# Optimization experiments

Hardware: AMD Instinct MI355X
Metric: run time of the kernel (lower is better)

The kernel has to match this reference:

```python
import jax, jax.numpy as jnp
import numpy as np

NX = NY = NZ = 192
DX = DY = DZ = 1e-3
DT = 1e-12
EPS0 = 8.8541878128e-12
MU0 = 1.25663706212e-6


def _dcentral(f, axis, inv2d):
    # central difference along `axis`, defined only on the interior of ALL
    # three dims (matches the torch edge lists built for i,j,k in 1..n-2);
    # boundary entries are zero (no scatter contributions there).
    g = jnp.zeros_like(f)
    sp = [slice(1, -1)] * 3
    sm = [slice(1, -1)] * 3
    sp[axis] = slice(2, None)
    sm[axis] = slice(0, -2)
    return g.at[1:-1, 1:-1, 1:-1].set((f[tuple(sp)] - f[tuple(sm)]) * inv2d)


def setup_inputs() -> dict:
    key = jax.random.key(0)
    ks = jax.random.split(key, 9)
    shp = (1, 1, NX, NY, NZ)
    f32 = jnp.float32
    inp = {}
    for name, k in zip(['Ex', 'Ey', 'Ez', 'Hx', 'Hy', 'Hz'], ks[:6]):
        inp[name] = jax.random.normal(k, shp, dtype=f32)
    inp['eps'] = (EPS0 * (1.0 + jax.random.uniform(ks[6], shp))).astype(f32)
    inp['mu'] = (MU0 * (1.0 + jax.random.uniform(ks[7], shp))).astype(f32)
    inp['sigma'] = (1e-3 * jax.random.uniform(ks[8], shp)).astype(f32)
    return inp


def reference(Ex, Ey, Ez, Hx, Hy, Hz, eps, mu, sigma):
    inv2dx = 1.0 / (2.0 * DX)
    inv2dy = 1.0 / (2.0 * DY)
    inv2dz = 1.0 / (2.0 * DZ)
    r3 = lambda a: a.reshape(NX, NY, NZ)  # _flatten3 equivalent layout
    ex, ey, ez = r3(Ex), r3(Ey), r3(Ez)
    hx, hy, hz = r3(Hx), r3(Hy), r3(Hz)
    eps3, mu3, sig3 = r3(eps), r3(mu), r3(sigma)

    # Step 1 (E -> H): H^{n+1/2} = H^{n-1/2} - dt/mu * curl(E^n)
    curlE_x = _dcentral(ez, 1, inv2dy) - _dcentral(ey, 2, inv2dz)
    curlE_y = _dcentral(ex, 2, inv2dz) - _dcentral(ez, 0, inv2dx)
    curlE_z = _dcentral(ey, 0, inv2dx) - _dcentral(ex, 1, inv2dy)
    hx2 = hx - (DT / mu3) * curlE_x
    hy2 = hy - (DT / mu3) * curlE_y
    hz2 = hz - (DT / mu3) * curlE_z

    # Step 2 (H -> E): E^{n+1} = (A-/A+) E^n + dt/(eps A+) * curl(H^{n+1/2})
    A_plus = 1.0 + sig3 * DT / (2.0 * eps3)
    A_minus = 1.0 - sig3 * DT / (2.0 * eps3)
    curlH_x = _dcentral(hz2, 1, inv2dy) - _dcentral(hy2, 2, inv2dz)
    curlH_y = _dcentral(hx2, 2, inv2dz) - _dcentral(hz2, 0, inv2dx)
    curlH_z = _dcentral(hy2, 0, inv2dx) - _dcentral(hx2, 1, inv2dy)
    coefE = A_minus / A_plus
    coefC = DT / (eps3 * A_plus)
    ex2 = coefE * ex + coefC * curlH_x
    ey2 = coefE * ey + coefC * curlH_y
    ez2 = coefE * ez + coefC * curlH_z

    u5 = lambda a: a.reshape(1, 1, NX, NY, NZ)  # _unflatten3
    return (u5(ex2), u5(ey2), u5(ez2), u5(hx2), u5(hy2), u5(hz2))
```

## Files before the change

kernel.cpp:

```cpp
#include <hip/hip_runtime.h>


#define NXD 192
#define NYD 192
#define NZD 192

static constexpr int   N3      = NXD * NYD * NZD;
static constexpr float DTc     = 1e-12f;
static constexpr float INV2D   = 500.0f;

static constexpr int SX = NYD * NZD;
static constexpr int SY = NZD;

__global__ __launch_bounds__(256) void fdtd_step1(
    const float* __restrict__ Ex, const float* __restrict__ Ey, const float* __restrict__ Ez,
    const float* __restrict__ Hx, const float* __restrict__ Hy, const float* __restrict__ Hz,
    const float* __restrict__ mu,
    float* __restrict__ Hx2, float* __restrict__ Hy2, float* __restrict__ Hz2)
{
    int idx = blockIdx.x * blockDim.x + threadIdx.x;
    if (idx >= N3) return;

    int k = idx % NZD;
    int t = idx / NZD;
    int j = t % NYD;
    int i = t / NYD;

    float cx = 0.0f, cy = 0.0f, cz = 0.0f;
    if (i > 0 && i < NXD - 1 && j > 0 && j < NYD - 1 && k > 0 && k < NZD - 1) {
        float dEz_dy = (Ez[idx + SY] - Ez[idx - SY]) * INV2D;
        float dEy_dz = (Ey[idx + 1 ] - Ey[idx - 1 ]) * INV2D;
        float dEx_dz = (Ex[idx + 1 ] - Ex[idx - 1 ]) * INV2D;
        float dEz_dx = (Ez[idx + SX] - Ez[idx - SX]) * INV2D;
        float dEy_dx = (Ey[idx + SX] - Ey[idx - SX]) * INV2D;
        float dEx_dy = (Ex[idx + SY] - Ex[idx - SY]) * INV2D;
        cx = dEz_dy - dEy_dz;
        cy = dEx_dz - dEz_dx;
        cz = dEy_dx - dEx_dy;
    }

    float f = DTc / mu[idx];
    Hx2[idx] = Hx[idx] - f * cx;
    Hy2[idx] = Hy[idx] - f * cy;
    Hz2[idx] = Hz[idx] - f * cz;
}

__global__ __launch_bounds__(256) void fdtd_step2(
    const float* __restrict__ Ex, const float* __restrict__ Ey, const float* __restrict__ Ez,
    const float* __restrict__ Hx2, const float* __restrict__ Hy2, const float* __restrict__ Hz2,
    const float* __restrict__ eps, const float* __restrict__ sigma,
    float* __restrict__ Ex2, float* __restrict__ Ey2, float* __restrict__ Ez2)
{
    int idx = blockIdx.x * blockDim.x + threadIdx.x;
    if (idx >= N3) return;

    int k = idx % NZD;
    int t = idx / NZD;
    int j = t % NYD;
    int i = t / NYD;

    float cx = 0.0f, cy = 0.0f, cz = 0.0f;
    if (i > 0 && i < NXD - 1 && j > 0 && j < NYD - 1 && k > 0 && k < NZD - 1) {
        float dHz_dy = (Hz2[idx + SY] - Hz2[idx - SY]) * INV2D;
        float dHy_dz = (Hy2[idx + 1 ] - Hy2[idx - 1 ]) * INV2D;
        float dHx_dz = (Hx2[idx + 1 ] - Hx2[idx - 1 ]) * INV2D;
        float dHz_dx = (Hz2[idx + SX] - Hz2[idx - SX]) * INV2D;
        float dHy_dx = (Hy2[idx + SX] - Hy2[idx - SX]) * INV2D;
        float dHx_dy = (Hx2[idx + SY] - Hx2[idx - SY]) * INV2D;
        cx = dHz_dy - dHy_dz;
        cy = dHx_dz - dHz_dx;
        cz = dHy_dx - dHx_dy;
    }

    float e  = eps[idx];
    float s  = sigma[idx];
    float half_sdt_over_e = s * DTc / (2.0f * e);
    float Ap = 1.0f + half_sdt_over_e;
    float Am = 1.0f - half_sdt_over_e;
    float coefE = Am / Ap;
    float coefC = DTc / (e * Ap);

    Ex2[idx] = coefE * Ex[idx] + coefC * cx;
    Ey2[idx] = coefE * Ey[idx] + coefC * cy;
    Ez2[idx] = coefE * Ez[idx] + coefC * cz;
}

extern "C" void kernel_launch(void* const* d_in, const int* in_sizes, int n_in,
                              void* d_out, int out_size, void* d_ws, size_t ws_size,
                              hipStream_t stream)
{
    const float* Ex    = (const float*)d_in[0];
    const float* Ey    = (const float*)d_in[1];
    const float* Ez    = (const float*)d_in[2];
    const float* Hx    = (const float*)d_in[3];
    const float* Hy    = (const float*)d_in[4];
    const float* Hz    = (const float*)d_in[5];
    const float* eps   = (const float*)d_in[6];
    const float* mu    = (const float*)d_in[7];
    const float* sigma = (const float*)d_in[8];

    float* out = (float*)d_out;
    float* Ex2 = out + 0 * (size_t)N3;
    float* Ey2 = out + 1 * (size_t)N3;
    float* Ez2 = out + 2 * (size_t)N3;
    float* Hx2 = out + 3 * (size_t)N3;
    float* Hy2 = out + 4 * (size_t)N3;
    float* Hz2 = out + 5 * (size_t)N3;

    const int block = 256;
    const int grid  = (N3 + block - 1) / block;

    fdtd_step1<<<grid, block, 0, stream>>>(Ex, Ey, Ez, Hx, Hy, Hz, mu, Hx2, Hy2, Hz2);
    fdtd_step2<<<grid, block, 0, stream>>>(Ex, Ey, Ez, Hx2, Hy2, Hz2, eps, sigma, Ex2, Ey2, Ez2);
}
```

Baseline: 379.5 us.

## Fuse H and E updates into one tiled kernel with shared-memory H halo

Merges the two stencil kernels into a single kernel where each block owns a 4x4 column tile along the full z extent. H updates for the tile plus a one-cell halo are computed into shared memory, then the E update reads curl(H) from shared memory instead of re-reading H2 from global memory. This removes the second launch and the global round-trip of the intermediate H fields, at the cost of redundant halo recomputation of H and its extra E/mu reads.

```diff
diff --git a/kernel.cpp b/kernel.cpp
--- a/kernel.cpp
+++ b/kernel.cpp
@@ -5,84 +5,148 @@
 #define NYD 192
 #define NZD 192
 
-static constexpr int   N3      = NXD * NYD * NZD;
-static constexpr float DTc     = 1e-12f;
-static constexpr float INV2D   = 500.0f;
+static constexpr int   N3    = NXD * NYD * NZD;
+static constexpr float DTc   = 1e-12f;
+static constexpr float INV2D = 500.0f;
 
 static constexpr int SX = NYD * NZD;
 static constexpr int SY = NZD;
 
-__global__ __launch_bounds__(256) void fdtd_step1(
+static constexpr int TI  = 4, TJ = 4;
+static constexpr int NTI = NXD / TI;
+static constexpr int NTJ = NYD / TJ;
+static constexpr int NT  = NTI * NTJ;
+static constexpr int BLOCK = 256;
+
+static constexpr int HZ_SZ = 6 * 6 * 192;
+static constexpr int HX_SZ = 4 * 6 * 194;
+static constexpr int HY_SZ = 6 * 4 * 194;
+
+__global__ __launch_bounds__(BLOCK, 2) void fdtd_fused(
     const float* __restrict__ Ex, const float* __restrict__ Ey, const float* __restrict__ Ez,
     const float* __restrict__ Hx, const float* __restrict__ Hy, const float* __restrict__ Hz,
-    const float* __restrict__ mu,
+    const float* __restrict__ eps, const float* __restrict__ mu, const float* __restrict__ sigma,
+    float* __restrict__ Ex2, float* __restrict__ Ey2, float* __restrict__ Ez2,
     float* __restrict__ Hx2, float* __restrict__ Hy2, float* __restrict__ Hz2)
 {
-    int idx = blockIdx.x * blockDim.x + threadIdx.x;
-    if (idx >= N3) return;
+    __shared__ float sHz[HZ_SZ];
+    __shared__ float sHx[HX_SZ];
+    __shared__ float sHy[HY_SZ];
 
-    int k = idx % NZD;
-    int t = idx / NZD;
-    int j = t % NYD;
-    int i = t / NYD;
+    unsigned b    = blockIdx.x;
+    unsigned tile = (b & 7u) * (NT / 8) + (b >> 3);
+    int ti = (int)(tile / NTJ);
+    int tj = (int)(tile % NTJ);
+    int gi0 = ti * TI;
+    int gj0 = tj * TJ;
 
-    float cx = 0.0f, cy = 0.0f, cz = 0.0f;
-    if (i > 0 && i < NXD - 1 && j > 0 && j < NYD - 1 && k > 0 && k < NZD - 1) {
-        float dEz_dy = (Ez[idx + SY] - Ez[idx - SY]) * INV2D;
-        float dEy_dz = (Ey[idx + 1 ] - Ey[idx - 1 ]) * INV2D;
-        float dEx_dz = (Ex[idx + 1 ] - Ex[idx - 1 ]) * INV2D;
-        float dEz_dx = (Ez[idx + SX] - Ez[idx - SX]) * INV2D;
-        float dEy_dx = (Ey[idx + SX] - Ey[idx - SX]) * INV2D;
-        float dEx_dy = (Ex[idx + SY] - Ex[idx - SY]) * INV2D;
-        cx = dEz_dy - dEy_dz;
-        cy = dEx_dz - dEz_dx;
-        cz = dEy_dx - dEx_dy;
+    const int tid = threadIdx.x;
+
+    for (int p = tid; p < HZ_SZ; p += BLOCK) {
+        int k  = p % 192;
+        int t  = p / 192;
+        int jj = t % 6;
+        int ii = t / 6;
+        int i = gi0 + ii - 1;
+        int j = gj0 + jj - 1;
+        if ((unsigned)i < (unsigned)NXD && (unsigned)j < (unsigned)NYD) {
+            int g = i * SX + j * SY + k;
+            float curl = 0.0f;
+            if (i > 0 && i < NXD - 1 && j > 0 && j < NYD - 1 && k > 0 && k < NZD - 1) {
+                curl = ((Ey[g + SX] - Ey[g - SX]) - (Ex[g + SY] - Ex[g - SY])) * INV2D;
+            }
+            float v = Hz[g] - (DTc / mu[g]) * curl;
+            sHz[p] = v;
+            if ((unsigned)(ii - 1) < (unsigned)TI && (unsigned)(jj - 1) < (unsigned)TJ)
+                Hz2[g] = v;
+        }
     }
 
-    float f = DTc / mu[idx];
-    Hx2[idx] = Hx[idx] - f * cx;
-    Hy2[idx] = Hy[idx] - f * cy;
-    Hz2[idx] = Hz[idx] - f * cz;
-}
-
-__global__ __launch_bounds__(256) void fdtd_step2(
-    const float* __restrict__ Ex, const float* __restrict__ Ey, const float* __restrict__ Ez,
-    const float* __restrict__ Hx2, const float* __restrict__ Hy2, const float* __restrict__ Hz2,
-    const float* __restrict__ eps, const float* __restrict__ sigma,
-    float* __restrict__ Ex2, float* __restrict__ Ey2, float* __restrict__ Ez2)
-{
-    int idx = blockIdx.x * blockDim.x + threadIdx.x;
-    if (idx >= N3) return;
-
-    int k = idx % NZD;
-    int t = idx / NZD;
-    int j = t % NYD;
-    int i = t / NYD;
-
-    float cx = 0.0f, cy = 0.0f, cz = 0.0f;
-    if (i > 0 && i < NXD - 1 && j > 0 && j < NYD - 1 && k > 0 && k < NZD - 1) {
-        float dHz_dy = (Hz2[idx + SY] - Hz2[idx - SY]) * INV2D;
-        float dHy_dz = (Hy2[idx + 1 ] - Hy2[idx - 1 ]) * INV2D;
-        float dHx_dz = (Hx2[idx + 1 ] - Hx2[idx - 1 ]) * INV2D;
-        float dHz_dx = (Hz2[idx + SX] - Hz2[idx - SX]) * INV2D;
-        float dHy_dx = (Hy2[idx + SX] - Hy2[idx - SX]) * INV2D;
-        float dHx_dy = (Hx2[idx + SY] - Hx2[idx - SY]) * INV2D;
-        cx = dHz_dy - dHy_dz;
-        cy = dHx_dz - dHz_dx;
-        cz = dHy_dx - dHx_dy;
+    for (int p = tid; p < HX_SZ; p += BLOCK) {
+        int kk = p % 194;
+        int t  = p / 194;
+        int jj = t % 6;
+        int ii = t / 6;
+        int i = gi0 + ii;
+        int j = gj0 + jj - 1;
+        int k = kk - 1;
+        if ((unsigned)j < (unsigned)NYD && (unsigned)k < (unsigned)NZD) {
+            int g = i * SX + j * SY + k;
+            float curl = 0.0f;
+            if (i > 0 && i < NXD - 1 && j > 0 && j < NYD - 1 && k > 0 && k < NZD - 1) {
+                curl = ((Ez[g + SY] - Ez[g - SY]) - (Ey[g + 1] - Ey[g - 1])) * INV2D;
+            }
+            float v = Hx[g] - (DTc / mu[g]) * curl;
+            sHx[p] = v;
+            if ((unsigned)(jj - 1) < (unsigned)TJ)
+                Hx2[g] = v;
+        }
     }
 
-    float e  = eps[idx];
-    float s  = sigma[idx];
-    float half_sdt_over_e = s * DTc / (2.0f * e);
-    float Ap = 1.0f + half_sdt_over_e;
-    float Am = 1.0f - half_sdt_over_e;
-    float coefE = Am / Ap;
-    float coefC = DTc / (e * Ap);
+    for (int p = tid; p < HY_SZ; p += BLOCK) {
+        int kk = p % 194;
+        int t  = p / 194;
+        int jj = t % 4;
+        int ii = t / 4;
+        int i = gi0 + ii - 1;
+        int j = gj0 + jj;
+        int k = kk - 1;
+        if ((unsigned)i < (unsigned)NXD && (unsigned)k < (unsigned)NZD) {
+            int g = i * SX + j * SY + k;
+            float curl = 0.0f;
+            if (i > 0 && i < NXD - 1 && j > 0 && j < NYD - 1 && k > 0 && k < NZD - 1) {
+                curl = ((Ex[g + 1] - Ex[g - 1]) - (Ez[g + SX] - Ez[g - SX])) * INV2D;
+            }
+            float v = Hy[g] - (DTc / mu[g]) * curl;
+            sHy[p] = v;
+            if ((unsigned)(ii - 1) < (unsigned)TI)
+                Hy2[g] = v;
+        }
+    }
 
-    Ex2[idx] = coefE * Ex[idx] + coefC * cx;
-    Ey2[idx] = coefE * Ey[idx] + coefC * cy;
-    Ez2[idx] = coefE * Ez[idx] + coefC * cz;
+    __syncthreads();
+
+    for (int p = tid; p < TI * TJ * 192; p += BLOCK) {
+        int k  = p % 192;
+        int t  = p / 192;
+        int jj = t % TJ;
+        int ii = t / TJ;
+        int i = gi0 + ii;
+        int j = gj0 + jj;
+        int g = i * SX + j * SY + k;
+
+        float cx = 0.0f, cy = 0.0f, cz = 0.0f;
+        if (i > 0 && i < NXD - 1 && j > 0 && j < NYD - 1 && k > 0 && k < NZD - 1) {
+            float dHzdy = sHz[((ii + 1) * 6 + (jj + 2)) * 192 + k]
+                        - sHz[((ii + 1) * 6 + (jj    )) * 192 + k];
+            float dHydz = sHy[((ii + 1) * 4 + jj) * 194 + (k + 2)]
+                        - sHy[((ii + 1) * 4 + jj) * 194 + (k    )];
+            cx = (dHzdy - dHydz) * INV2D;
+
+            float dHxdz = sHx[(ii * 6 + (jj + 1)) * 194 + (k + 2)]
+                        - sHx[(ii * 6 + (jj + 1)) * 194 + (k    )];
+            float dHzdx = sHz[((ii + 2) * 6 + (jj + 1)) * 192 + k]
+                        - sHz[((ii    ) * 6 + (jj + 1)) * 192 + k];
+            cy = (dHxdz - dHzdx) * INV2D;
+
+            float dHydx = sHy[((ii + 2) * 4 + jj) * 194 + (k + 1)]
+                        - sHy[((ii    ) * 4 + jj) * 194 + (k + 1)];
+            float dHxdy = sHx[(ii * 6 + (jj + 2)) * 194 + (k + 1)]
+                        - sHx[(ii * 6 + (jj    )) * 194 + (k + 1)];
+            cz = (dHydx - dHxdy) * INV2D;
+        }
+
+        float e  = eps[g];
+        float sg = sigma[g];
+        float hs = sg * (0.5f * DTc) / e;
+        float r  = 1.0f / (1.0f + hs);
+        float cE = (1.0f - hs) * r;
+        float cC = DTc * r / e;
+
+        Ex2[g] = cE * Ex[g] + cC * cx;
+        Ey2[g] = cE * Ey[g] + cC * cy;
+        Ez2[g] = cE * Ez[g] + cC * cz;
+    }
 }
 
 extern "C" void kernel_launch(void* const* d_in, const int* in_sizes, int n_in,
@@ -107,9 +171,6 @@
     float* Hy2 = out + 4 * (size_t)N3;
     float* Hz2 = out + 5 * (size_t)N3;
 
-    const int block = 256;
-    const int grid  = (N3 + block - 1) / block;
-
-    fdtd_step1<<<grid, block, 0, stream>>>(Ex, Ey, Ez, Hx, Hy, Hz, mu, Hx2, Hy2, Hz2);
-    fdtd_step2<<<grid, block, 0, stream>>>(Ex, Ey, Ez, Hx2, Hy2, Hz2, eps, sigma, Ex2, Ey2, Ez2);
+    fdtd_fused<<<NT, BLOCK, 0, stream>>>(Ex, Ey, Ez, Hx, Hy, Hz, eps, mu, sigma,
+                                         Ex2, Ey2, Ez2, Hx2, Hy2, Hz2);
 }
```

New measurement: 640.6 us. 68.8% more time.
